# Kernel tuning notes

Measured on AMD Instinct MI355X. Metric: run time of the kernel, lower is better.

Reference implementation:

```python
import jax, jax.numpy as jnp
import numpy as np

B, S, D, H, L, K = 16, 384, 512, 8, 4, 7
HD = D // H
MAXLEN = 400


def _pos_encoding(d=D, max_len=MAXLEN):
    # Faithful to the (unusual) torch loop: even idx i -> sin(pos/10000**(2i/d)),
    # odd idx i+1 -> cos(pos/10000**(2(i+1)/d))
    pe = np.zeros((max_len, d), dtype=np.float32)
    pos = np.arange(max_len, dtype=np.float64)[:, None]
    i = np.arange(0, d, 2)
    pe[:, i] = np.sin(pos / 10000.0 ** (2 * i / d))
    pe[:, i + 1] = np.cos(pos / 10000.0 ** (2 * (i + 1) / d))
    return jnp.asarray(pe)

POS_ENC = _pos_encoding()


def layer_norm(x, g, b, eps=1e-5):
    m = jnp.mean(x, -1, keepdims=True)
    v = jnp.mean((x - m) ** 2, -1, keepdims=True)
    return (x - m) * jax.lax.rsqrt(v + eps) * g + b


def dsconv(x, dw_w, pw_w, pw_b):
    # x: [B,S,D]; depthwise conv1d (no bias) then pointwise 1x1 (bias)
    xc = jnp.transpose(x, (0, 2, 1))  # [B,D,S]
    y = jax.lax.conv_general_dilated(
        xc, dw_w, window_strides=(1,), padding=[(K // 2, K // 2)],
        dimension_numbers=("NCH", "OIH", "NCH"), feature_group_count=D)  # [B,D,S]
    return jnp.einsum("bcs,oc->bso", y, pw_w) + pw_b  # [B,S,D]


def setup_inputs():
    key = jax.random.key(0)
    ks = jax.random.split(key, 16)
    sc = 0.02
    inp = {
        "x": jax.random.normal(ks[0], (B, S, D), jnp.float32),
        "mask": jax.random.randint(ks[1], (B, S), 0, 2, jnp.int32),
        "dw_w": jax.random.normal(ks[2], (L, D, 1, K), jnp.float32) * sc,
        "pw_w": jax.random.normal(ks[3], (L, D, D), jnp.float32) * sc,
        "pw_b": jnp.zeros((L, D), jnp.float32),
        "conv_ln_g": jnp.ones((L, D), jnp.float32),
        "conv_ln_b": jnp.zeros((L, D), jnp.float32),
        "pos_ln_g": jnp.ones((D,), jnp.float32),
        "pos_ln_b": jnp.zeros((D,), jnp.float32),
        "wq": jax.random.normal(ks[4], (D, D), jnp.float32) * sc,
        "bq": jnp.zeros((D,), jnp.float32),
        "wk": jax.random.normal(ks[5], (D, D), jnp.float32) * sc,
        "bk": jnp.zeros((D,), jnp.float32),
        "wv": jax.random.normal(ks[6], (D, D), jnp.float32) * sc,
        "bv": jnp.zeros((D,), jnp.float32),
        "wo": jax.random.normal(ks[7], (D, D), jnp.float32) * sc,
        "bo": jnp.zeros((D,), jnp.float32),
        "ff_ln_g": jnp.ones((D,), jnp.float32),
        "ff_ln_b": jnp.zeros((D,), jnp.float32),
        "ff_w": jax.random.normal(ks[8], (D, D), jnp.float32) * sc,
        "ff_b": jnp.zeros((D,), jnp.float32),
    }
    return inp


def attention(x, mask, wq, bq, wk, bk, wv, bv, wo, bo):
    def heads(w, b):
        y = jnp.einsum("bsd,od->bso", x, w) + b
        return jnp.transpose(y.reshape(B, S, H, HD), (0, 2, 1, 3))  # [B,H,S,HD]
    q, k, v = heads(wq, bq), heads(wk, bk), heads(wv, bv)
    energy = jnp.einsum("bhqd,bhkd->bhqk", q, k) / jnp.sqrt(jnp.float32(HD))
    m = (mask == 1)[:, None, None, :]  # [B,1,1,S]
    energy = jnp.where(m, jnp.float32(-1e10), energy)
    alpha = jax.nn.softmax(energy, axis=-1)  # dropout = identity (eval)
    a = jnp.einsum("bhqk,bhkd->bhqd", alpha, v)
    a = jnp.transpose(a, (0, 2, 1, 3)).reshape(B, S, D)
    return jnp.einsum("bsd,od->bso", a, wo) + bo


def reference(x, mask, dw_w, pw_w, pw_b, conv_ln_g, conv_ln_b, pos_ln_g, pos_ln_b,
              wq, bq, wk, bk, wv, bv, wo, bo, ff_ln_g, ff_ln_b, ff_w, ff_b):
    out = x + POS_ENC[None, :S, :]
    res = out
    out = layer_norm(out, pos_ln_g, pos_ln_b)
    for i in range(L):
        out = jax.nn.relu(dsconv(out, dw_w[i], pw_w[i], pw_b[i]))
        out = out + res  # dropout = identity (eval)
        res = out
        out = layer_norm(out, conv_ln_g[i], conv_ln_b[i])
    out = attention(out, mask, wq, bq, wk, bk, wv, bv, wo, bo)
    out = out + res
    res = out
    out = layer_norm(out, ff_ln_g, ff_ln_b)
    out = jax.nn.relu(jnp.einsum("bsd,od->bso", out, ff_w) + ff_b)
    return out + res
```

## Files before the change

kernel.cpp:

```cpp
#include <hip/hip_runtime.h>

#define BB 16
#define SS 384
#define DD 512
#define HH 8
#define HDIM 64
#define LLAY 4
#define KW 7
#define MM (BB*SS)

typedef unsigned short u16;
typedef unsigned int u32;
typedef short short8v __attribute__((ext_vector_type(8)));
typedef float floatx4 __attribute__((ext_vector_type(4)));

__device__ __forceinline__ float bf2f(u16 u) {
    union { u32 i; float f; } v; v.i = ((u32)u) << 16; return v.f;
}
__device__ __forceinline__ u16 f2bf(float f) {
    union { float f; u32 i; } v; v.f = f;
    return (u16)((v.i + 0x7FFFu + ((v.i >> 16) & 1u)) >> 16);
}
__device__ __forceinline__ bool sniff_f32(const void* dtp) {
    return *((const u32*)dtp) == 0x3F800000u;
}
__device__ __forceinline__ float ldf(const void* p, long i, bool f32) {
    return f32 ? ((const float*)p)[i] : bf2f(((const u16*)p)[i]);
}
__device__ __forceinline__ short8v ldfrag_scalar(const void* p, long i, bool f32) {
    short8v r;
    if (f32) {
        const float* q = (const float*)p + i;
#pragma unroll
        for (int j = 0; j < 8; j++) r[j] = (short)f2bf(q[j]);
    } else {
        r = *(const short8v*)((const u16*)p + i);
    }
    return r;
}

__device__ __forceinline__ void load_lds16(const u16* g, u16* l) {
    __builtin_amdgcn_global_load_lds((const __attribute__((address_space(1))) void*)g,
                                     (__attribute__((address_space(3))) void*)l, 16, 0, 0);
}
__device__ __forceinline__ int swz(int row) { return (row & 3) ^ ((row >> 2) & 3); }
__device__ __forceinline__ short8v lds_frag(const u16* buf, int row, int quad) {
    return *(const short8v*)(buf + ((size_t)row * 4 + (quad ^ swz(row))) * 8);
}

__device__ __forceinline__ floatx4 mfma16(short8v a, short8v b, floatx4 c) {
    return __builtin_amdgcn_mfma_f32_16x16x32_bf16(a, b, c, 0, 0, 0);
}

#define WCV_DW 2359296
#define WCV_TOT (WCV_DW + LLAY*KW*DD)
#define NCVB ((WCV_TOT + 255) / 256)

__global__ __launch_bounds__(256) void posln_cvt_kernel(
    const void* __restrict__ x, const void* __restrict__ g, const void* __restrict__ bvec,
    u16* __restrict__ res, u16* __restrict__ out,
    const void* __restrict__ pw_w, const void* __restrict__ wq,
    const void* __restrict__ wk, const void* __restrict__ wv,
    const void* __restrict__ wo, const void* __restrict__ ff_w,
    const void* __restrict__ dw_w, u16* __restrict__ wdst,
    const void* __restrict__ dtp) {
    const bool f32 = sniff_f32(dtp);
    const int tid = threadIdx.x;
    if (blockIdx.x >= MM) {
        const int i = (blockIdx.x - MM) * 256 + tid;
        if (i >= WCV_TOT) return;
        const void* src; long idx;
        if (i < 1048576) { src = pw_w; idx = i; }
        else if (i < WCV_DW) {
            const int j = i - 1048576;
            const int m = j >> 18;
            idx = j & 262143;
            src = (m == 0) ? wq : (m == 1) ? wk : (m == 2) ? wv : (m == 3) ? wo : ff_w;
        } else {
            const int j = i - WCV_DW;
            const int l = j / (KW * DD);
            const int r1 = j % (KW * DD);
            const int t = r1 / DD, c = r1 % DD;
            src = dw_w; idx = ((long)l * DD + c) * KW + t;
        }
        wdst[i] = f2bf(ldf(src, idx, f32));
        return;
    }
    const int row = blockIdx.x;
    const int s = row % SS;
    float v[2];
#pragma unroll
    for (int i = 0; i < 2; i++) {
        const int d = tid + i * 256;
        const float freq = __expf(-(float)d * 0.035977892078032f);
        const float arg = (float)s * freq;
        const float pe = (d & 1) ? __cosf(arg) : __sinf(arg);
        v[i] = ldf(x, (long)row * DD + d, f32) + pe;
        res[row * DD + d] = f2bf(v[i]);
    }
    float sum = v[0] + v[1], sq = v[0] * v[0] + v[1] * v[1];
#pragma unroll
    for (int off = 32; off; off >>= 1) { sum += __shfl_down(sum, off); sq += __shfl_down(sq, off); }
    __shared__ float red[4][2];
    const int wv2 = tid >> 6;
    if ((tid & 63) == 0) { red[wv2][0] = sum; red[wv2][1] = sq; }
    __syncthreads();
    sum = red[0][0] + red[1][0] + red[2][0] + red[3][0];
    sq  = red[0][1] + red[1][1] + red[2][1] + red[3][1];
    const float mean = sum * (1.f / DD);
    const float rstd = rsqrtf(sq * (1.f / DD) - mean * mean + 1e-5f);
#pragma unroll
    for (int i = 0; i < 2; i++) {
        const int d = tid + i * 256;
        out[row * DD + d] = f2bf((v[i] - mean) * rstd * ldf(g, d, f32) + ldf(bvec, d, f32));
    }
}

__global__ __launch_bounds__(512) void lnres_kernel(const u16* __restrict__ y,
                                                    const void* __restrict__ g,
                                                    const void* __restrict__ bvec,
                                                    int blayer,
                                                    u16* __restrict__ out,
                                                    const void* __restrict__ dtp) {
    const bool f32 = sniff_f32(dtp);
    const long voff = (long)blayer * DD;
    const int row = blockIdx.x * 8 + (threadIdx.x >> 6);
    const int lane = threadIdx.x & 63;
    const short8v v = *(const short8v*)(y + (size_t)row * DD + lane * 8);
    float f[8], sum = 0.f, sq = 0.f;
#pragma unroll
    for (int j = 0; j < 8; j++) { f[j] = bf2f((u16)v[j]); sum += f[j]; sq += f[j] * f[j]; }
#pragma unroll
    for (int off = 32; off; off >>= 1) { sum += __shfl_xor(sum, off); sq += __shfl_xor(sq, off); }
    const float mean = sum * (1.f / DD);
    const float rstd = rsqrtf(sq * (1.f / DD) - mean * mean + 1e-5f);
    short8v o;
#pragma unroll
    for (int j = 0; j < 8; j++) {
        const int d = lane * 8 + j;
        o[j] = (short)f2bf((f[j] - mean) * rstd * ldf(g, voff + d, f32) + ldf(bvec, voff + d, f32));
    }
    *(short8v*)(out + (size_t)row * DD + lane * 8) = o;
}

template <int VEC>
__global__ __launch_bounds__(256) void dwconv_kernel(const u16* __restrict__ in,
                                                     const void* __restrict__ w, int layer,
                                                     u16* __restrict__ out,
                                                     const void* __restrict__ dtp) {
    if constexpr (VEC) {
        const int bsw = (blockIdx.x & 7) * (MM * DD / 8 / 256 / 8) + (blockIdx.x >> 3);
        const int idx = bsw * 256 + threadIdx.x;
        const int c8 = (idx & 63) * 8;
        const int ms = idx >> 6;
        const int s = ms % SS;
        const u16* wl = (const u16*)w + (size_t)layer * KW * DD;
        float acc[8] = {0, 0, 0, 0, 0, 0, 0, 0};
#pragma unroll
        for (int t = 0; t < KW; t++) {
            const int ss2 = s + t - 3;
            if (ss2 >= 0 && ss2 < SS) {
                const short8v iv = *(const short8v*)(in + (size_t)(ms + t - 3) * DD + c8);
                const short8v wv = *(const short8v*)(wl + t * DD + c8);
#pragma unroll
                for (int j = 0; j < 8; j++)
                    acc[j] += bf2f((u16)iv[j]) * bf2f((u16)wv[j]);
            }
        }
        short8v ov;
#pragma unroll
        for (int j = 0; j < 8; j++) ov[j] = (short)f2bf(acc[j]);
        *(short8v*)(out + (size_t)ms * DD + c8) = ov;
    } else {
        const bool f32 = sniff_f32(dtp);
        const long woff = (long)layer * DD * KW;
        const int idx = blockIdx.x * 256 + threadIdx.x;
        const int c = idx & (DD - 1);
        const int ms = idx >> 9;
        const int s = ms % SS;
        float acc = 0.f;
#pragma unroll
        for (int t = 0; t < KW; t++) {
            const int ss2 = s + t - 3;
            if (ss2 >= 0 && ss2 < SS)
                acc += bf2f(in[(ms + t - 3) * DD + c]) * ldf(w, woff + c * KW + t, f32);
        }
        out[idx] = f2bf(acc);
    }
}

__device__ __forceinline__ void stage64(const u16* A, const u16* Wp, int m0,
                                        u16* Ab, u16* Wb, int tid, int k0) {
#pragma unroll
    for (int j = 0; j < 2; j++) {
        const int c = j * 256 + tid;
        const int row = c >> 2;
        const int kp = (c & 3) ^ swz(row);
        load_lds16(Wp + (size_t)row * DD + k0 + kp * 8, Wb + (size_t)c * 8);
    }
    {
        const int row = tid >> 2;
        const int kp = (tid & 3) ^ swz(row);
        load_lds16(A + (size_t)(m0 + row) * DD + k0 + kp * 8, Ab + (size_t)tid * 8);
    }
}

__device__ __forceinline__ void kloop64(const u16* A, const u16* Wp, int m0,
                                        u16* Abuf, u16* Wbuf,
                                        int tid, int wm, int wn, int ln15, int quad,
                                        floatx4 acc[2][4]) {
    stage64(A, Wp, m0, Abuf, Wbuf, tid, 0);
    __syncthreads();
    for (int ks = 0; ks < 16; ks++) {
        const int cur = ks & 1;
        u16* Ab = Abuf + cur * (64 * 32);
        u16* Wb = Wbuf + cur * (128 * 32);
        if (ks < 15)
            stage64(A, Wp, m0, Abuf + (cur ^ 1) * (64 * 32),
                    Wbuf + (cur ^ 1) * (128 * 32), tid, (ks + 1) * 32);
        const short8v a0 = lds_frag(Ab, wm * 32 + ln15, quad);
        const short8v a1 = lds_frag(Ab, wm * 32 + 16 + ln15, quad);
#pragma unroll
        for (int nt = 0; nt < 4; nt++) {
            const short8v b = lds_frag(Wb, wn * 64 + nt * 16 + ln15, quad);
            acc[0][nt] = mfma16(a0, b, acc[0][nt]);
            acc[1][nt] = mfma16(a1, b, acc[1][nt]);
        }
        __syncthreads();
    }
}

template <int RELU, int FINAL>
__global__ __launch_bounds__(256, 4) void gemm64_kernel(
    const u16* __restrict__ A, const u16* __restrict__ W,
    const void* __restrict__ bias, int blayer,
    const u16* __restrict__ res_in, u16* __restrict__ res_out,
    void* __restrict__ out, const void* __restrict__ dtp) {
    const bool f32 = sniff_f32(dtp);
    const long voff = (long)blayer * DD;
    __shared__ __align__(16) u16 smem[12288];
    u16* Wbuf = smem;
    u16* Abuf = smem + 8192;
    const int tid = threadIdx.x;
    const int m0 = blockIdx.x * 64, n0 = blockIdx.y * 128;
    const int wave = tid >> 6, lane = tid & 63;
    const int wm = wave >> 1, wn = wave & 1;
    const int ln15 = lane & 15, quad = lane >> 4;

    floatx4 acc[2][4];
#pragma unroll
    for (int mt = 0; mt < 2; mt++)
#pragma unroll
        for (int nt = 0; nt < 4; nt++) acc[mt][nt] = {0.f, 0.f, 0.f, 0.f};

    kloop64(A, W + (size_t)n0 * DD, m0, Abuf, Wbuf, tid, wm, wn, ln15, quad, acc);

#pragma unroll
    for (int nt = 0; nt < 4; nt++) {
        const int col = n0 + wn * 64 + nt * 16 + ln15;
        const float bval = ldf(bias, voff + col, f32);
#pragma unroll
        for (int mt = 0; mt < 2; mt++)
#pragma unroll
            for (int r = 0; r < 4; r++) {
                const int m = m0 + wm * 32 + mt * 16 + quad * 4 + r;
                float y = acc[mt][nt][r] + bval;
                if (RELU) y = fmaxf(y, 0.f);
                y += bf2f(res_in[(size_t)m * DD + col]);
                if (res_out) res_out[(size_t)m * DD + col] = f2bf(y);
                if constexpr (FINAL) {
                    if (f32) ((float*)out)[(size_t)m * DD + col] = y;
                    else     ((u16*)out)[(size_t)m * DD + col] = f2bf(y);
                }
            }
    }
}

#define VP 72
__global__ __launch_bounds__(256, 4) void qkv64_kernel(
    const u16* __restrict__ A,
    const u16* __restrict__ Wq, const u16* __restrict__ Wk, const u16* __restrict__ Wv,
    const void* __restrict__ bq, const void* __restrict__ bk, const void* __restrict__ bv,
    u16* __restrict__ qo, u16* __restrict__ ko, u16* __restrict__ vo,
    const void* __restrict__ dtp) {
    const bool f32 = sniff_f32(dtp);
    const int sel = blockIdx.z;
    const u16* W = (sel == 0) ? Wq : (sel == 1) ? Wk : Wv;
    const void* bias = (sel == 0) ? bq : (sel == 1) ? bk : bv;

    __shared__ __align__(16) u16 smem[12288];
    u16* Wbuf = smem;
    u16* Abuf = smem + 8192;
    u16 (*vtile)[VP] = (u16 (*)[VP])smem;

    const int tid = threadIdx.x;
    const int m0 = blockIdx.x * 64, n0 = blockIdx.y * 128;
    const int wave = tid >> 6, lane = tid & 63;
    const int wm = wave >> 1, wn = wave & 1;
    const int ln15 = lane & 15, quad = lane >> 4;
    const int bidx = m0 / SS;

    floatx4 acc[2][4];
#pragma unroll
    for (int mt = 0; mt < 2; mt++)
#pragma unroll
        for (int nt = 0; nt < 4; nt++) acc[mt][nt] = {0.f, 0.f, 0.f, 0.f};

    kloop64(A, W + (size_t)n0 * DD, m0, Abuf, Wbuf, tid, wm, wn, ln15, quad, acc);

    if (sel == 2) {
#pragma unroll
        for (int nt = 0; nt < 4; nt++) {
            const int cl = wn * 64 + nt * 16 + ln15;
            const float bval = ldf(bias, n0 + cl, f32);
#pragma unroll
            for (int mt = 0; mt < 2; mt++)
#pragma unroll
                for (int r = 0; r < 4; r++)
                    vtile[cl][wm * 32 + mt * 16 + quad * 4 + r] = f2bf(acc[mt][nt][r] + bval);
        }
        __syncthreads();
        const int c = tid & 127, half = tid >> 7;
        const int col = n0 + c;
        const int h = col >> 6, hd = col & 63;
        u16* dst = vo + ((size_t)(bidx * HH + h) * HDIM + hd) * SS
                      + (m0 - bidx * SS) + half * 32;
        const u16* srcl = &vtile[c][half * 32];
#pragma unroll
        for (int j = 0; j < 4; j++)
            *(short8v*)(dst + j * 8) = *(const short8v*)(srcl + j * 8);
    } else {
        u16* out = (sel == 0) ? qo : ko;
#pragma unroll
        for (int nt = 0; nt < 4; nt++) {
            const int col = n0 + wn * 64 + nt * 16 + ln15;
            const int h = col >> 6, hd = col & 63;
            const float bval = ldf(bias, col, f32);
#pragma unroll
            for (int mt = 0; mt < 2; mt++)
#pragma unroll
                for (int r = 0; r < 4; r++) {
                    const int m = m0 + wm * 32 + mt * 16 + quad * 4 + r;
                    const int s = m - bidx * SS;
                    out[((size_t)(bidx * HH + h) * SS + s) * HDIM + hd] = f2bf(acc[mt][nt][r] + bval);
                }
        }
    }
}

template <int RELU, int DO_LN, int FINAL>
__global__ __launch_bounds__(512, 4) void gemm16_kernel(
    const u16* __restrict__ A, const void* __restrict__ W, int wlayer,
    const void* __restrict__ bias, const void* __restrict__ g,
    const void* __restrict__ bvec, int blayer,
    const u16* __restrict__ res_in, u16* __restrict__ res_out,
    void* __restrict__ out, const void* __restrict__ dtp) {
    const bool f32 = sniff_f32(dtp);
    const long woff = (long)wlayer * DD * DD;
    const long voff = (long)blayer * DD;
    __shared__ float part[8][16][2];
    const int tid = threadIdx.x;
    const int m0 = blockIdx.x * 16;
    const int wave = tid >> 6, lane = tid & 63;
    const int ln15 = lane & 15, quad = lane >> 4;

    floatx4 acc[4];
#pragma unroll
    for (int nt = 0; nt < 4; nt++) acc[nt] = {0.f, 0.f, 0.f, 0.f};

    const u16* A0 = A + (size_t)(m0 + ln15) * DD + quad * 8;
#pragma unroll
    for (int ks = 0; ks < 16; ks++) {
        const int k0 = ks * 32;
        short8v a0 = *(const short8v*)(A0 + k0);
        short8v b[4];
#pragma unroll
        for (int nt = 0; nt < 4; nt++) {
            const long wrow = woff + (long)(wave * 64 + nt * 16 + ln15) * DD + quad * 8 + k0;
            b[nt] = ldfrag_scalar(W, wrow, f32);
        }
#pragma unroll
        for (int nt = 0; nt < 4; nt++)
            acc[nt] = mfma16(a0, b[nt], acc[nt]);
    }

#pragma unroll
    for (int nt = 0; nt < 4; nt++) {
        const int col = wave * 64 + nt * 16 + ln15;
        const float bval = ldf(bias, voff + col, f32);
#pragma unroll
        for (int r = 0; r < 4; r++) {
            const int m = m0 + quad * 4 + r;
            float y = acc[nt][r] + bval;
            if (RELU) y = fmaxf(y, 0.f);
            y += bf2f(res_in[(size_t)m * DD + col]);
            if (res_out) res_out[(size_t)m * DD + col] = f2bf(y);
            acc[nt][r] = y;
        }
    }
    if constexpr (DO_LN) {
        float ls[4], lq[4];
#pragma unroll
        for (int r = 0; r < 4; r++) {
            float s = 0.f, q = 0.f;
#pragma unroll
            for (int nt = 0; nt < 4; nt++) { const float y = acc[nt][r]; s += y; q += y * y; }
            ls[r] = s; lq[r] = q;
        }
#pragma unroll
        for (int off = 1; off < 16; off <<= 1)
#pragma unroll
            for (int r = 0; r < 4; r++) {
                ls[r] += __shfl_xor(ls[r], off);
                lq[r] += __shfl_xor(lq[r], off);
            }
        if (ln15 == 0) {
#pragma unroll
            for (int r = 0; r < 4; r++) {
                part[wave][quad * 4 + r][0] = ls[r];
                part[wave][quad * 4 + r][1] = lq[r];
            }
        }
        __syncthreads();
        float mean[4], rstd[4];
#pragma unroll
        for (int r = 0; r < 4; r++) {
            const int rr = quad * 4 + r;
            float s = 0.f, q = 0.f;
#pragma unroll
            for (int wv = 0; wv < 8; wv++) { s += part[wv][rr][0]; q += part[wv][rr][1]; }
            const float mn = s * (1.f / DD);
            mean[r] = mn;
            rstd[r] = rsqrtf(q * (1.f / DD) - mn * mn + 1e-5f);
        }
#pragma unroll
        for (int nt = 0; nt < 4; nt++) {
            const int col = wave * 64 + nt * 16 + ln15;
            const float gv = ldf(g, voff + col, f32);
            const float bv = ldf(bvec, voff + col, f32);
#pragma unroll
            for (int r = 0; r < 4; r++) {
                const int m = m0 + quad * 4 + r;
                ((u16*)out)[(size_t)m * DD + col] =
                    f2bf((acc[nt][r] - mean[r]) * rstd[r] * gv + bv);
            }
        }
    } else {
#pragma unroll
        for (int nt = 0; nt < 4; nt++) {
            const int col = wave * 64 + nt * 16 + ln15;
#pragma unroll
            for (int r = 0; r < 4; r++) {
                const int m = m0 + quad * 4 + r;
                if (FINAL && f32) ((float*)out)[(size_t)m * DD + col] = acc[nt][r];
                else              ((u16*)out)[(size_t)m * DD + col] = f2bf(acc[nt][r]);
            }
        }
    }
}

__global__ __launch_bounds__(512, 4) void qkv16_kernel(
    const u16* __restrict__ A,
    const void* __restrict__ Wq, const void* __restrict__ Wk, const void* __restrict__ Wv,
    const void* __restrict__ bq, const void* __restrict__ bk, const void* __restrict__ bv,
    u16* __restrict__ qo, u16* __restrict__ ko, u16* __restrict__ vo,
    const void* __restrict__ dtp) {
    const bool f32 = sniff_f32(dtp);
    const int sel = blockIdx.y;
    const void* W = (sel == 0) ? Wq : (sel == 1) ? Wk : Wv;
    const void* bias = (sel == 0) ? bq : (sel == 1) ? bk : bv;

    const int tid = threadIdx.x;
    const int m0 = blockIdx.x * 16;
    const int wave = tid >> 6, lane = tid & 63;
    const int ln15 = lane & 15, quad = lane >> 4;
    const int bidx = m0 / SS;

    floatx4 acc[4];
#pragma unroll
    for (int nt = 0; nt < 4; nt++) acc[nt] = {0.f, 0.f, 0.f, 0.f};

    const u16* A0 = A + (size_t)(m0 + ln15) * DD + quad * 8;
#pragma unroll
    for (int ks = 0; ks < 16; ks++) {
        const int k0 = ks * 32;
        short8v a0 = *(const short8v*)(A0 + k0);
        short8v b[4];
#pragma unroll
        for (int nt = 0; nt < 4; nt++) {
            const long wrow = (long)(wave * 64 + nt * 16 + ln15) * DD + quad * 8 + k0;
            b[nt] = ldfrag_scalar(W, wrow, f32);
        }
#pragma unroll
        for (int nt = 0; nt < 4; nt++)
            acc[nt] = mfma16(a0, b[nt], acc[nt]);
    }

    if (sel == 2) {
#pragma unroll
        for (int nt = 0; nt < 4; nt++) {
            const int col = wave * 64 + nt * 16 + ln15;
            const int h = col >> 6, hd = col & 63;
            const float bval = ldf(bias, col, f32);
#pragma unroll
            for (int r = 0; r < 4; r++) {
                const int m = m0 + quad * 4 + r;
                const int s = m - bidx * SS;
                vo[((size_t)(bidx * HH + h) * HDIM + hd) * SS + s] = f2bf(acc[nt][r] + bval);
            }
        }
    } else {
        u16* out = (sel == 0) ? qo : ko;
#pragma unroll
        for (int nt = 0; nt < 4; nt++) {
            const int col = wave * 64 + nt * 16 + ln15;
            const int h = col >> 6, hd = col & 63;
            const float bval = ldf(bias, col, f32);
#pragma unroll
            for (int r = 0; r < 4; r++) {
                const int m = m0 + quad * 4 + r;
                const int s = m - bidx * SS;
                out[((size_t)(bidx * HH + h) * SS + s) * HDIM + hd] = f2bf(acc[nt][r] + bval);
            }
        }
    }
}

#define ALP 392
__global__ __launch_bounds__(256) void attn_kernel(const u16* __restrict__ q,
                                                   const u16* __restrict__ k,
                                                   const u16* __restrict__ vT,
                                                   const int* __restrict__ mask,
                                                   u16* __restrict__ out) {
    __shared__ __align__(16) u16 Kb[3072 * 8];
    __shared__ __align__(16) u16 Vb[3072 * 8];
    __shared__ __align__(16) u16 al4[4][16][ALP];

    const int n = blockIdx.x;
    const int i = n >> 3;
    const int g = (n & 7) * 16 + i / 6;
    const int sub = i % 6;
    const int h = g & 7, b = g >> 3;
    const int tid = threadIdx.x;
    const int wave = tid >> 6, lane = tid & 63;
    const int ln15 = lane & 15, quad = lane >> 4;
    const int q0 = (sub * 4 + wave) * 16;

    const u16* qh = q + (size_t)(b * HH + h) * SS * HDIM;
    const u16* kh = k + (size_t)(b * HH + h) * SS * HDIM;
    const u16* vh = vT + (size_t)(b * HH + h) * HDIM * SS;

#pragma unroll
    for (int j = 0; j < 12; j++) {
        const int c = j * 256 + tid;
        const int row = c >> 3, cc = c & 7;
        const int kp = cc ^ ((row ^ (row >> 3)) & 7);
        load_lds16(kh + (size_t)row * HDIM + kp * 8, Kb + (size_t)c * 8);
    }
#pragma unroll
    for (int j = 0; j < 12; j++) {
        const int c = j * 256 + tid;
        const int tile = c >> 8, rr = (c >> 2) & 63, cc = c & 3;
        const int kp = cc ^ swz(rr);
        load_lds16(vh + (size_t)rr * SS + tile * 32 + kp * 8, Vb + (size_t)c * 8);
    }
    const short8v* arow = (const short8v*)(qh + (q0 + ln15) * HDIM + quad * 8);
    const short8v a0 = arow[0], a1 = arow[4];
    __syncthreads();

    floatx4 sc[24];
#pragma unroll
    for (int t = 0; t < 24; t++) {
        const int row = t * 16 + ln15;
        const int s3 = (row ^ (row >> 3)) & 7;
        const short8v b0 = *(const short8v*)(Kb + ((size_t)row * 8 + (quad ^ s3)) * 8);
        const short8v b1 = *(const short8v*)(Kb + ((size_t)row * 8 + ((4 + quad) ^ s3)) * 8);
        floatx4 acc = {0.f, 0.f, 0.f, 0.f};
        acc = mfma16(a0, b0, acc);
        acc = mfma16(a1, b1, acc);
        sc[t] = acc;
    }
    float mx[4] = {-3.0e38f, -3.0e38f, -3.0e38f, -3.0e38f};
#pragma unroll
    for (int t = 0; t < 24; t++) {
        const bool msk = (mask[b * SS + t * 16 + ln15] == 1);
#pragma unroll
        for (int r = 0; r < 4; r++) {
            float v = sc[t][r] * 0.125f;
            if (msk) v = -1e10f;
            sc[t][r] = v;
            mx[r] = fmaxf(mx[r], v);
        }
    }
#pragma unroll
    for (int off = 8; off; off >>= 1)
#pragma unroll
        for (int r = 0; r < 4; r++) mx[r] = fmaxf(mx[r], __shfl_xor(mx[r], off, 16));
    float sum[4] = {0.f, 0.f, 0.f, 0.f};
    u16* alw = &al4[wave][0][0];
#pragma unroll
    for (int t = 0; t < 24; t++) {
#pragma unroll
        for (int r = 0; r < 4; r++) {
            const float p = __expf(sc[t][r] - mx[r]);
            sum[r] += p;
            alw[(quad * 4 + r) * ALP + t * 16 + ln15] = f2bf(p);
        }
    }
#pragma unroll
    for (int off = 8; off; off >>= 1)
#pragma unroll
        for (int r = 0; r < 4; r++) sum[r] += __shfl_xor(sum[r], off, 16);
    __builtin_amdgcn_s_waitcnt(0);

#pragma unroll
    for (int dt = 0; dt < 4; dt++) {
        floatx4 acc = {0.f, 0.f, 0.f, 0.f};
        const int row = dt * 16 + ln15;
        const int vsw = quad ^ swz(row);
#pragma unroll
        for (int c2 = 0; c2 < 12; c2++) {
            const short8v af = *(const short8v*)(alw + ln15 * ALP + c2 * 32 + quad * 8);
            const short8v bf = *(const short8v*)(Vb + ((size_t)c2 * 256 + row * 4 + vsw) * 8);
            acc = mfma16(af, bf, acc);
        }
#pragma unroll
        for (int rr = 0; rr < 4; rr++) {
            const int s = q0 + quad * 4 + rr;
            out[((size_t)(b * SS + s)) * DD + h * HDIM + dt * 16 + ln15] = f2bf(acc[rr] / sum[rr]);
        }
    }
}

extern "C" void kernel_launch(void* const* d_in, const int* in_sizes, int n_in,
                              void* d_out, int out_size, void* d_ws, size_t ws_size,
                              hipStream_t stream) {
    (void)in_sizes; (void)n_in; (void)out_size;
    const void* x     = d_in[0];
    const int*  mask  = (const int*)d_in[1];
    const void* dw_w  = d_in[2];
    const void* pw_w  = d_in[3];
    const void* pw_b  = d_in[4];
    const void* cln_g = d_in[5];
    const void* cln_b = d_in[6];
    const void* pln_g = d_in[7];
    const void* pln_b = d_in[8];
    const void* wq    = d_in[9];
    const void* bq    = d_in[10];
    const void* wk    = d_in[11];
    const void* bk    = d_in[12];
    const void* wv    = d_in[13];
    const void* bv    = d_in[14];
    const void* wo    = d_in[15];
    const void* bo    = d_in[16];
    const void* fln_g = d_in[17];
    const void* fln_b = d_in[18];
    const void* ff_w  = d_in[19];
    const void* ff_b  = d_in[20];
    const void* dtp   = cln_g;

    const size_t nAct = (size_t)MM * DD;
    char* p = (char*)d_ws;
    u16* res   = (u16*)p; p += nAct * 2;
    u16* lnout = (u16*)p; p += nAct * 2;
    u16* tmp   = (u16*)p; p += nAct * 2;
    u16* vT    = (u16*)p; p += nAct * 2;
    u16* wcv   = (u16*)p;
    u16* kb    = (u16*)d_out;

    const size_t needFast = nAct * 2 * 4 + (size_t)WCV_TOT * 2;
    const bool fast = (ws_size >= needFast);

    if (fast) {
        posln_cvt_kernel<<<MM + NCVB, 256, 0, stream>>>(
            x, pln_g, pln_b, res, lnout,
            pw_w, wq, wk, wv, wo, ff_w, dw_w, wcv, dtp);
        const u16* w_pw = wcv;
        const u16* w_q  = wcv + 1048576;
        const u16* w_k  = wcv + 1310720;
        const u16* w_v  = wcv + 1572864;
        const u16* w_o  = wcv + 1835008;
        const u16* w_ff = wcv + 2097152;
        const u16* w_dw = wcv + WCV_DW;

        for (int i = 0; i < LLAY; i++) {
            dwconv_kernel<1><<<MM * DD / 8 / 256, 256, 0, stream>>>(lnout, w_dw, i, tmp, dtp);
            gemm64_kernel<1, 0><<<dim3(MM / 64, 4), 256, 0, stream>>>(
                tmp, w_pw + (size_t)i * DD * DD, pw_b, i, res, res, nullptr, dtp);
            lnres_kernel<<<MM / 8, 512, 0, stream>>>(res, cln_g, cln_b, i, lnout, dtp);
        }
        qkv64_kernel<<<dim3(MM / 64, 4, 3), 256, 0, stream>>>(
            lnout, w_q, w_k, w_v, bq, bk, bv, tmp, kb, vT, dtp);

        attn_kernel<<<BB * HH * (SS / 64), 256, 0, stream>>>(tmp, kb, vT, mask, lnout);

        gemm64_kernel<0, 0><<<dim3(MM / 64, 4), 256, 0, stream>>>(
            lnout, w_o, bo, 0, res, res, nullptr, dtp);
        lnres_kernel<<<MM / 8, 512, 0, stream>>>(res, fln_g, fln_b, 0, lnout, dtp);
        gemm64_kernel<1, 1><<<dim3(MM / 64, 4), 256, 0, stream>>>(
            lnout, w_ff, ff_b, 0, res, nullptr, d_out, dtp);
    } else {
        posln_cvt_kernel<<<MM, 256, 0, stream>>>(
            x, pln_g, pln_b, res, lnout,
            pw_w, wq, wk, wv, wo, ff_w, dw_w, (u16*)d_ws, dtp);
        for (int i = 0; i < LLAY; i++) {
            dwconv_kernel<0><<<MM * DD / 256, 256, 0, stream>>>(lnout, dw_w, i, tmp, dtp);
            gemm16_kernel<1, 1, 0><<<MM / 16, 512, 0, stream>>>(
                tmp, pw_w, i, pw_b, cln_g, cln_b, i, res, res, lnout, dtp);
        }
        qkv16_kernel<<<dim3(MM / 16, 3), 512, 0, stream>>>(
            lnout, wq, wk, wv, bq, bk, bv, tmp, kb, vT, dtp);

        attn_kernel<<<BB * HH * (SS / 64), 256, 0, stream>>>(tmp, kb, vT, mask, lnout);

        gemm16_kernel<0, 1, 0><<<MM / 16, 512, 0, stream>>>(
            lnout, wo, 0, bo, fln_g, fln_b, 0, res, res, lnout, dtp);
        gemm16_kernel<1, 0, 1><<<MM / 16, 512, 0, stream>>>(
            lnout, ff_w, 0, ff_b, nullptr, nullptr, 0, res, nullptr, d_out, dtp);
    }
}
```

Baseline: 333.5 us.

## Fuse layernorm into depthwise conv and relax GEMM k-loop barriers

Adds a dwln kernel that loads 14 residual rows (8 outputs plus a 3-row halo on each side) into LDS, applies the layernorm in place, then runs the 7-tap depthwise conv from LDS. This removes the separate lnres launch and the round trip of the normalized activations through global memory for each conv layer. Halo rows are layer-normalized redundantly, and rows clamped at the array edges rely on the sequence-boundary check. Separately, the GEMM k-loop replaces __syncthreads with explicit vmcnt/lgkmcnt waits plus s_barrier, so the next tile's global loads can stay in flight while the current tile is computed.

```diff
diff --git a/kernel.cpp b/kernel.cpp
--- a/kernel.cpp
+++ b/kernel.cpp
@@ -143,50 +143,87 @@
     *(short8v*)(out + (size_t)row * DD + lane * 8) = o;
 }
 
-template <int VEC>
+__global__ __launch_bounds__(256) void dwln_kernel(
+    const u16* __restrict__ res, const u16* __restrict__ wdw ,
+    const void* __restrict__ g, const void* __restrict__ bvec, int voff,
+    u16* __restrict__ out, const void* __restrict__ dtp) {
+    const bool f32 = sniff_f32(dtp);
+    __shared__ __align__(16) u16 rows[14][DD];
+    const int tid = threadIdx.x;
+    const int lane = tid & 63, wave = tid >> 6;
+    const int m0 = blockIdx.x * 8;
+#pragma unroll
+    for (int j = 0; j < 4; j++) {
+        const int c = j * 256 + tid;
+        if (c < 896) {
+            int gr = m0 - 3 + (c >> 6);
+            gr = (gr < 0) ? 0 : (gr >= MM ? MM - 1 : gr);
+            load_lds16(res + (size_t)gr * DD + (c & 63) * 8, &rows[0][0] + (size_t)c * 8);
+        }
+    }
+    float gv[8], bv[8];
+#pragma unroll
+    for (int e = 0; e < 8; e++) {
+        gv[e] = ldf(g, (long)voff + lane * 8 + e, f32);
+        bv[e] = ldf(bvec, (long)voff + lane * 8 + e, f32);
+    }
+    asm volatile("s_waitcnt vmcnt(0)\n\ts_barrier" ::: "memory");
+    for (int j = wave; j < 14; j += 4) {
+        const short8v v = *(const short8v*)&rows[j][lane * 8];
+        float f[8], s = 0.f, q = 0.f;
+#pragma unroll
+        for (int e = 0; e < 8; e++) { f[e] = bf2f((u16)v[e]); s += f[e]; q += f[e] * f[e]; }
+#pragma unroll
+        for (int off = 32; off; off >>= 1) { s += __shfl_xor(s, off); q += __shfl_xor(q, off); }
+        const float mean = s * (1.f / DD);
+        const float rstd = rsqrtf(q * (1.f / DD) - mean * mean + 1e-5f);
+        short8v o;
+#pragma unroll
+        for (int e = 0; e < 8; e++) o[e] = (short)f2bf((f[e] - mean) * rstd * gv[e] + bv[e]);
+        *(short8v*)&rows[j][lane * 8] = o;
+    }
+    asm volatile("s_waitcnt lgkmcnt(0)\n\ts_barrier" ::: "memory");
+    short8v wv[KW];
+#pragma unroll
+    for (int t = 0; t < KW; t++) wv[t] = *(const short8v*)(wdw + t * DD + lane * 8);
+#pragma unroll
+    for (int rr = wave; rr < 8; rr += 4) {
+        const int gm = m0 + rr, s = gm % SS;
+        float acc[8] = {0, 0, 0, 0, 0, 0, 0, 0};
+#pragma unroll
+        for (int t = 0; t < KW; t++) {
+            const int ss2 = s + t - 3;
+            if (ss2 >= 0 && ss2 < SS) {
+                const short8v iv = *(const short8v*)&rows[rr + t][lane * 8];
+#pragma unroll
+                for (int e = 0; e < 8; e++) acc[e] += bf2f((u16)iv[e]) * bf2f((u16)wv[t][e]);
+            }
+        }
+        short8v ov;
+#pragma unroll
+        for (int e = 0; e < 8; e++) ov[e] = (short)f2bf(acc[e]);
+        *(short8v*)(out + (size_t)gm * DD + lane * 8) = ov;
+    }
+}
+
 __global__ __launch_bounds__(256) void dwconv_kernel(const u16* __restrict__ in,
                                                      const void* __restrict__ w, int layer,
                                                      u16* __restrict__ out,
                                                      const void* __restrict__ dtp) {
-    if constexpr (VEC) {
-        const int bsw = (blockIdx.x & 7) * (MM * DD / 8 / 256 / 8) + (blockIdx.x >> 3);
-        const int idx = bsw * 256 + threadIdx.x;
-        const int c8 = (idx & 63) * 8;
-        const int ms = idx >> 6;
-        const int s = ms % SS;
-        const u16* wl = (const u16*)w + (size_t)layer * KW * DD;
-        float acc[8] = {0, 0, 0, 0, 0, 0, 0, 0};
-#pragma unroll
-        for (int t = 0; t < KW; t++) {
-            const int ss2 = s + t - 3;
-            if (ss2 >= 0 && ss2 < SS) {
-                const short8v iv = *(const short8v*)(in + (size_t)(ms + t - 3) * DD + c8);
-                const short8v wv = *(const short8v*)(wl + t * DD + c8);
-#pragma unroll
-                for (int j = 0; j < 8; j++)
-                    acc[j] += bf2f((u16)iv[j]) * bf2f((u16)wv[j]);
-            }
-        }
-        short8v ov;
-#pragma unroll
-        for (int j = 0; j < 8; j++) ov[j] = (short)f2bf(acc[j]);
-        *(short8v*)(out + (size_t)ms * DD + c8) = ov;
-    } else {
-        const bool f32 = sniff_f32(dtp);
-        const long woff = (long)layer * DD * KW;
-        const int idx = blockIdx.x * 256 + threadIdx.x;
-        const int c = idx & (DD - 1);
-        const int ms = idx >> 9;
-        const int s = ms % SS;
-        float acc = 0.f;
-#pragma unroll
-        for (int t = 0; t < KW; t++) {
-            const int ss2 = s + t - 3;
-            if (ss2 >= 0 && ss2 < SS)
-                acc += bf2f(in[(ms + t - 3) * DD + c]) * ldf(w, woff + c * KW + t, f32);
-        }
-        out[idx] = f2bf(acc);
-    }
+    const bool f32 = sniff_f32(dtp);
+    const long woff = (long)layer * DD * KW;
+    const int idx = blockIdx.x * 256 + threadIdx.x;
+    const int c = idx & (DD - 1);
+    const int ms = idx >> 9;
+    const int s = ms % SS;
+    float acc = 0.f;
+#pragma unroll
+    for (int t = 0; t < KW; t++) {
+        const int ss2 = s + t - 3;
+        if (ss2 >= 0 && ss2 < SS)
+            acc += bf2f(in[(ms + t - 3) * DD + c]) * ldf(w, woff + c * KW + t, f32);
+    }
+    out[idx] = f2bf(acc);
 }
 
 __device__ __forceinline__ void stage64(const u16* A, const u16* Wp, int m0,
@@ -210,14 +247,17 @@
                                         int tid, int wm, int wn, int ln15, int quad,
                                         floatx4 acc[2][4]) {
     stage64(A, Wp, m0, Abuf, Wbuf, tid, 0);
-    __syncthreads();
     for (int ks = 0; ks < 16; ks++) {
         const int cur = ks & 1;
         u16* Ab = Abuf + cur * (64 * 32);
         u16* Wb = Wbuf + cur * (128 * 32);
-        if (ks < 15)
+        if (ks < 15) {
             stage64(A, Wp, m0, Abuf + (cur ^ 1) * (64 * 32),
                     Wbuf + (cur ^ 1) * (128 * 32), tid, (ks + 1) * 32);
+            asm volatile("s_waitcnt vmcnt(3)\n\ts_barrier" ::: "memory");
+        } else {
+            asm volatile("s_waitcnt vmcnt(0)\n\ts_barrier" ::: "memory");
+        }
         const short8v a0 = lds_frag(Ab, wm * 32 + ln15, quad);
         const short8v a1 = lds_frag(Ab, wm * 32 + 16 + ln15, quad);
 #pragma unroll
@@ -226,7 +266,7 @@
             acc[0][nt] = mfma16(a0, b, acc[0][nt]);
             acc[1][nt] = mfma16(a1, b, acc[1][nt]);
         }
-        __syncthreads();
+        asm volatile("s_waitcnt lgkmcnt(0)\n\ts_barrier" ::: "memory");
     }
 }
 
@@ -684,11 +724,15 @@
         const u16* w_dw = wcv + WCV_DW;
 
         for (int i = 0; i < LLAY; i++) {
-            dwconv_kernel<1><<<MM * DD / 8 / 256, 256, 0, stream>>>(lnout, w_dw, i, tmp, dtp);
+            const void* lg = (i == 0) ? pln_g : cln_g;
+            const void* lb = (i == 0) ? pln_b : cln_b;
+            const int lo = (i == 0) ? 0 : (i - 1) * DD;
+            dwln_kernel<<<MM / 8, 256, 0, stream>>>(
+                res, w_dw + (size_t)i * KW * DD, lg, lb, lo, tmp, dtp);
             gemm64_kernel<1, 0><<<dim3(MM / 64, 4), 256, 0, stream>>>(
                 tmp, w_pw + (size_t)i * DD * DD, pw_b, i, res, res, nullptr, dtp);
-            lnres_kernel<<<MM / 8, 512, 0, stream>>>(res, cln_g, cln_b, i, lnout, dtp);
-        }
+        }
+        lnres_kernel<<<MM / 8, 512, 0, stream>>>(res, cln_g, cln_b, LLAY - 1, lnout, dtp);
         qkv64_kernel<<<dim3(MM / 64, 4, 3), 256, 0, stream>>>(
             lnout, w_q, w_k, w_v, bq, bk, bv, tmp, kb, vT, dtp);
 
@@ -704,7 +748,7 @@
             x, pln_g, pln_b, res, lnout,
             pw_w, wq, wk, wv, wo, ff_w, dw_w, (u16*)d_ws, dtp);
         for (int i = 0; i < LLAY; i++) {
-            dwconv_kernel<0><<<MM * DD / 256, 256, 0, stream>>>(lnout, dw_w, i, tmp, dtp);
+            dwconv_kernel<<<MM * DD / 256, 256, 0, stream>>>(lnout, dw_w, i, tmp, dtp);
             gemm16_kernel<1, 1, 0><<<MM / 16, 512, 0, stream>>>(
                 tmp, pw_w, i, pw_b, cln_g, cln_b, i, res, res, lnout, dtp);
         }
```

Result: faster. 324.9 us (-2.6%).
